# Optimization experiments

Measured on AMD Instinct MI355X. Metric: run time of the kernel, lower is better.

The kernel has to match this reference:

```python
import jax, jax.numpy as jnp
import numpy as np


def setup_inputs() -> dict:
    key = jax.random.key(0)
    k1, k2, k3, k4 = jax.random.split(key, 4)
    B, C_ORIG, H, W = 64, 448, 56, 56
    C = 100
    P = H * W
    feats = jax.random.normal(k1, (B, C_ORIG, H, W), dtype=jnp.float32)
    mean = jax.random.normal(k2, (P, C), dtype=jnp.float32)
    icov = jax.random.normal(k3, (P, C, C), dtype=jnp.float32)
    sel_idx = jnp.sort(jax.random.randint(k4, (C,), 0, C_ORIG, dtype=jnp.int64))
    return {"feats": feats, "mean": mean, "icov": icov, "sel_idx": sel_idx,
            "image_size": 224}


def reference(feats, mean, icov, sel_idx, image_size):
    # feats: [B, C_orig, H, W]; select the PaDiM random channel subset -> [B, C, H, W]
    f = feats[:, sel_idx]
    B, C, H, W = f.shape
    # [B, H*W, C] patch-major layout as in the torch code
    f = jnp.transpose(f, (0, 2, 3, 1)).reshape(B, H * W, C)
    # Per-patch Mahalanobis distance, fully batched over all H*W patches
    # (replaces the Python loop of H*W small einsums in the original).
    diff = f - mean[None]                                   # [B, P, C]
    dist = jnp.einsum('bpi,pij,bpj->bp', diff, icov, diff)  # [B, P]
    score_map = dist.reshape(B, H, W)
    # Bilinear upsample to input resolution (align_corners=False ~ half-pixel)
    score_map = jax.image.resize(score_map, (B, image_size, image_size),
                                 method='bilinear')
    return score_map
```

## Files before the change

### kernel.cpp

```cpp
#include <hip/hip_runtime.h>
#include <hip/hip_bf16.h>

#define B_N     64
#define C_ORIG  448
#define C_SEL   100
#define CP      128
#define HW      3136
#define IMG     224

typedef short bf16x8 __attribute__((ext_vector_type(8)));
typedef float f32x4  __attribute__((ext_vector_type(4)));

static __device__ __forceinline__ unsigned short f2bf(float f) {
    unsigned int u = __float_as_uint(f);
    return (unsigned short)((u + 0x7FFFu + ((u >> 16) & 1u)) >> 16);
}
static __device__ __forceinline__ float bf2f(unsigned short h) {
    return __uint_as_float(((unsigned int)h) << 16);
}

__global__ __launch_bounds__(256) void kA_gather(const float* __restrict__ feats,
                                                 const float* __restrict__ mean,
                                                 const int* __restrict__ sel,
                                                 unsigned short* __restrict__ D)
{
    __shared__ unsigned short Dt[64 * 128];
    char* DtB = reinterpret_cast<char*>(Dt);
    const int tid = threadIdx.x;
    const int p0  = blockIdx.x * 64;
    const int b   = blockIdx.y;

#pragma unroll
    for (int q = 0; q < 2; ++q) {
        int z = tid + q * 256;
        if (z < 448) {
            int pr = z / 7, un = 25 + z % 7;
            *reinterpret_cast<uint2*>(DtB + pr * 256 + ((8 * un) ^ ((pr & 31) << 3)))
                = make_uint2(0u, 0u);
        }
    }

    const int w    = tid >> 6;
    const int lane = tid & 63;
    const float* fb   = feats + (size_t)b * (C_ORIG * HW) + p0 + lane;
    const float* mrow = mean + (size_t)(p0 + lane) * C_SEL;
    const unsigned swz = (unsigned)(lane & 31) << 3;
    char* rowB = DtB + lane * 256;

    auto quad = [&](int c0) {
        int ch0 = sel[c0], ch1 = sel[c0 + 1], ch2 = sel[c0 + 2], ch3 = sel[c0 + 3];
        float4 m4 = *reinterpret_cast<const float4*>(mrow + c0);
        float v0 = fb[(size_t)ch0 * HW] - m4.x;
        float v1 = fb[(size_t)ch1 * HW] - m4.y;
        float v2 = fb[(size_t)ch2 * HW] - m4.z;
        float v3 = fb[(size_t)ch3 * HW] - m4.w;
        uint2 pk = make_uint2((unsigned)f2bf(v0) | ((unsigned)f2bf(v1) << 16),
                              (unsigned)f2bf(v2) | ((unsigned)f2bf(v3) << 16));
        *reinterpret_cast<uint2*>(rowB + (((unsigned)(2 * c0)) ^ swz)) = pk;
    };

    if (w < 3) {
#pragma unroll
        for (int q = 0; q < 6; ++q) quad(w * 24 + q * 4);
    } else {
#pragma unroll
        for (int q = 0; q < 7; ++q) quad(72 + q * 4);
    }
    __syncthreads();

    unsigned short* Dp = D + (size_t)p0 * (B_N * CP) + (size_t)b * CP;
#pragma unroll
    for (int q = 0; q < 4; ++q) {
        int unit = tid + q * 256;
        int pr = unit >> 4;
        int s  = unit & 15;
        unsigned off = ((unsigned)(16 * s)) ^ ((((unsigned)pr & 31u) << 3) & 0xF0u);
        uint4 v = *reinterpret_cast<const uint4*>(DtB + pr * 256 + off);
        uint4 r = (pr & 1) ? make_uint4(v.z, v.w, v.x, v.y) : v;
        *reinterpret_cast<uint4*>(reinterpret_cast<char*>(Dp)
            + (size_t)pr * (B_N * CP * 2) + s * 16) = r;
    }
}

__global__ __launch_bounds__(256) void kB_maha(const float* __restrict__ icov,
                                               const unsigned short* __restrict__ D,
                                               float* __restrict__ dist)
{
    __shared__ unsigned short Mb[112 * 128];
    char* MbB = reinterpret_cast<char*>(Mb);
    const int tid = threadIdx.x;
    const int p   = blockIdx.x;
    const int w    = tid >> 6;
    const int lane = tid & 63;
    const int lrow = lane & 15;
    const int g    = lane >> 4;
    const int bcol = w * 16 + lrow;
    const unsigned short* Drow = D + (size_t)p * (B_N * CP) + (size_t)bcol * CP;

    bf16x8 bfr[4];
#pragma unroll
    for (int ks = 0; ks < 4; ++ks)
        bfr[ks] = *reinterpret_cast<const bf16x8*>(Drow + ks * 32 + g * 8);
    ushort4 dvec[7];
#pragma unroll
    for (int it = 0; it < 7; ++it)
        dvec[it] = *reinterpret_cast<const ushort4*>(Drow + it * 16 + g * 4);

#pragma unroll
    for (int q = 0; q < 3; ++q) {
        int z = tid + q * 256;
        if (z < 700) {
            int i = z / 7, un = 25 + z % 7;
            *reinterpret_cast<uint2*>(MbB + i * 256 + ((8 * un) ^ ((i & 7) << 4)))
                = make_uint2(0u, 0u);
        }
    }
#pragma unroll
    for (int q = 0; q < 2; ++q) {
        int z = tid + q * 256;
        if (z < 384) {
            int i = 100 + (z >> 5), un = z & 31;
            *reinterpret_cast<uint2*>(MbB + i * 256 + ((8 * un) ^ ((i & 7) << 4)))
                = make_uint2(0u, 0u);
        }
    }
    const float4* src = reinterpret_cast<const float4*>(icov + (size_t)p * (C_SEL * C_SEL));
#pragma unroll
    for (int q = 0; q < 10; ++q) {
        int idx4 = tid + q * 256;
        if (idx4 < 2500) {
            float4 v = src[idx4];
            int i = idx4 / 25, un = idx4 % 25;
            uint2 pk = make_uint2((unsigned)f2bf(v.x) | ((unsigned)f2bf(v.y) << 16),
                                  (unsigned)f2bf(v.z) | ((unsigned)f2bf(v.w) << 16));
            *reinterpret_cast<uint2*>(MbB + i * 256 + ((8 * un) ^ ((i & 7) << 4))) = pk;
        }
    }
    __syncthreads();

    f32x4 acc[7];
#pragma unroll
    for (int it = 0; it < 7; ++it) acc[it] = (f32x4){0.f, 0.f, 0.f, 0.f};

#pragma unroll
    for (int ks = 0; ks < 4; ++ks) {
#pragma unroll
        for (int it = 0; it < 7; ++it) {
            int i = it * 16 + lrow;
            bf16x8 afrag = *reinterpret_cast<const bf16x8*>(
                MbB + i * 256 + ((ks * 64 + g * 16) ^ ((i & 7) << 4)));
            acc[it] = __builtin_amdgcn_mfma_f32_16x16x32_bf16(afrag, bfr[ks], acc[it], 0, 0, 0);
        }
    }

    float partial = 0.f;
#pragma unroll
    for (int it = 0; it < 7; ++it) {
#pragma unroll
        for (int r = 0; r < 4; ++r) {
            int i = it * 16 + g * 4 + r;
            if (i < C_SEL) {
                unsigned short dh = (r == 0) ? dvec[it].x : (r == 1) ? dvec[it].y
                                   : (r == 2) ? dvec[it].z : dvec[it].w;
                partial += acc[it][r] * bf2f(dh);
            }
        }
    }
    partial += __shfl_xor(partial, 16);
    partial += __shfl_xor(partial, 32);
    if (g == 0) dist[p * B_N + bcol] = partial;
}

__global__ __launch_bounds__(256) void kC_resize(const float* __restrict__ dist,
                                                 float* __restrict__ out)
{
    int gid = blockIdx.x * 256 + threadIdx.x;
    int m = gid % 56;
    int t = gid / 56;
    int y = t % IMG;
    int b = t / IMG;

    float sy = y * 0.25f - 0.375f;
    float fy0 = floorf(sy);
    float fy = sy - fy0;
    int y0 = max((int)fy0, 0);
    int y1 = min((int)fy0 + 1, 55);
    int xm1 = max(m - 1, 0);
    int xp1 = min(m + 1, 55);

    const float* d0 = dist + (y0 * 56) * B_N + b;
    const float* d1 = dist + (y1 * 56) * B_N + b;
    float a0 = d0[xm1 * B_N], b0 = d0[m * B_N], c0 = d0[xp1 * B_N];
    float a1 = d1[xm1 * B_N], b1 = d1[m * B_N], c1 = d1[xp1 * B_N];

    float A  = a0 + fy * (a1 - a0);
    float Bv = b0 + fy * (b1 - b0);
    float Cv = c0 + fy * (c1 - c0);

    float4 o;
    o.x = A  + 0.625f * (Bv - A);
    o.y = A  + 0.875f * (Bv - A);
    o.z = Bv + 0.125f * (Cv - Bv);
    o.w = Bv + 0.375f * (Cv - Bv);
    *reinterpret_cast<float4*>(out + ((size_t)b * IMG + y) * IMG + 4 * m) = o;
}

extern "C" void kernel_launch(void* const* d_in, const int* in_sizes, int n_in,
                              void* d_out, int out_size, void* d_ws, size_t ws_size,
                              hipStream_t stream)
{
    const float* feats = (const float*)d_in[0];
    const float* mean  = (const float*)d_in[1];
    const float* icov  = (const float*)d_in[2];
    const int*   sel   = (const int*)d_in[3];
    float* out = (float*)d_out;

    unsigned short* Dws = (unsigned short*)d_ws;
    float* distws = (float*)((char*)d_ws + (size_t)HW * B_N * CP * 2);

    dim3 gA(49, B_N);
    kA_gather<<<gA, 256, 0, stream>>>(feats, mean, sel, Dws);
    kB_maha<<<HW, 256, 0, stream>>>(icov, Dws, distws);
    kC_resize<<<3136, 256, 0, stream>>>(distws, out);
}
```

Before: 87.22 us.

## Load icov fragments directly into MFMA registers and shrink D padding

The Mahalanobis kernel no longer stages each patch's 100x100 icov into shared memory. Each lane now loads its own row fragments from global memory, converts them to bf16 in registers and feeds the MFMA directly, which removes the LDS fill, the barrier and the shared-memory footprint so more blocks fit per CU (launch bounds set to 4). The diff buffer padding drops from 128 to 112 channels to cut workspace traffic, and the distance output is stored batch-major so the resize kernel reads contiguous rows. In exchange, the icov global loads are less coalesced (per-lane 16-byte row pieces) and nothing overlaps them with compute.

```diff
diff --git a/kernel.cpp b/kernel.cpp
--- a/kernel.cpp
+++ b/kernel.cpp
@@ -4,16 +4,18 @@
 #define B_N     64
 #define C_ORIG  448
 #define C_SEL   100
-#define CP      128
+#define CPD     112
 #define HW      3136
 #define IMG     224
 
 typedef short bf16x8 __attribute__((ext_vector_type(8)));
 typedef float f32x4  __attribute__((ext_vector_type(4)));
-
-static __device__ __forceinline__ unsigned short f2bf(float f) {
-    unsigned int u = __float_as_uint(f);
-    return (unsigned short)((u + 0x7FFFu + ((u >> 16) & 1u)) >> 16);
+typedef unsigned int u32x4 __attribute__((ext_vector_type(4)));
+
+static __device__ __forceinline__ unsigned pkbf(float x, float y) {
+    union { __hip_bfloat162 h; unsigned u; } c;
+    c.h = __float22bfloat162_rn(float2{x, y});
+    return c.u;
 }
 static __device__ __forceinline__ float bf2f(unsigned short h) {
     return __uint_as_float(((unsigned int)h) << 16);
@@ -30,14 +32,10 @@
     const int p0  = blockIdx.x * 64;
     const int b   = blockIdx.y;
 
-#pragma unroll
-    for (int q = 0; q < 2; ++q) {
-        int z = tid + q * 256;
-        if (z < 448) {
-            int pr = z / 7, un = 25 + z % 7;
-            *reinterpret_cast<uint2*>(DtB + pr * 256 + ((8 * un) ^ ((pr & 31) << 3)))
-                = make_uint2(0u, 0u);
-        }
+    if (tid < 192) {
+        int pr = tid / 3, un = 25 + tid % 3;
+        *reinterpret_cast<uint2*>(DtB + pr * 256 + ((8 * un) ^ ((pr & 31) << 3)))
+            = make_uint2(0u, 0u);
     }
 
     const int w    = tid >> 6;
@@ -54,8 +52,7 @@
         float v1 = fb[(size_t)ch1 * HW] - m4.y;
         float v2 = fb[(size_t)ch2 * HW] - m4.z;
         float v3 = fb[(size_t)ch3 * HW] - m4.w;
-        uint2 pk = make_uint2((unsigned)f2bf(v0) | ((unsigned)f2bf(v1) << 16),
-                              (unsigned)f2bf(v2) | ((unsigned)f2bf(v3) << 16));
+        uint2 pk = make_uint2(pkbf(v0, v1), pkbf(v2, v3));
         *reinterpret_cast<uint2*>(rowB + (((unsigned)(2 * c0)) ^ swz)) = pk;
     };
 
@@ -68,34 +65,34 @@
     }
     __syncthreads();
 
-    unsigned short* Dp = D + (size_t)p0 * (B_N * CP) + (size_t)b * CP;
+    unsigned short* Dp = D + ((size_t)p0 * B_N + b) * CPD;
 #pragma unroll
     for (int q = 0; q < 4; ++q) {
         int unit = tid + q * 256;
-        int pr = unit >> 4;
-        int s  = unit & 15;
-        unsigned off = ((unsigned)(16 * s)) ^ ((((unsigned)pr & 31u) << 3) & 0xF0u);
-        uint4 v = *reinterpret_cast<const uint4*>(DtB + pr * 256 + off);
-        uint4 r = (pr & 1) ? make_uint4(v.z, v.w, v.x, v.y) : v;
-        *reinterpret_cast<uint4*>(reinterpret_cast<char*>(Dp)
-            + (size_t)pr * (B_N * CP * 2) + s * 16) = r;
-    }
-}
-
-__global__ __launch_bounds__(256) void kB_maha(const float* __restrict__ icov,
-                                               const unsigned short* __restrict__ D,
-                                               float* __restrict__ dist)
-{
-    __shared__ unsigned short Mb[112 * 128];
-    char* MbB = reinterpret_cast<char*>(Mb);
-    const int tid = threadIdx.x;
-    const int p   = blockIdx.x;
+        if (unit < 896) {
+            int pr = unit / 14;
+            int s  = unit % 14;
+            unsigned off = ((unsigned)(16 * s)) ^ ((((unsigned)pr & 31u) << 3) & 0xF0u);
+            uint4 v = *reinterpret_cast<const uint4*>(DtB + pr * 256 + off);
+            uint4 r = (pr & 1) ? make_uint4(v.z, v.w, v.x, v.y) : v;
+            *reinterpret_cast<uint4*>(reinterpret_cast<char*>(Dp)
+                + (size_t)pr * (B_N * CPD * 2) + s * 16) = r;
+        }
+    }
+}
+
+__global__ __launch_bounds__(256, 4) void kB_maha(const float* __restrict__ icov,
+                                                  const unsigned short* __restrict__ D,
+                                                  float* __restrict__ dist)
+{
+    const int tid  = threadIdx.x;
+    const int p    = blockIdx.x;
     const int w    = tid >> 6;
     const int lane = tid & 63;
     const int lrow = lane & 15;
     const int g    = lane >> 4;
     const int bcol = w * 16 + lrow;
-    const unsigned short* Drow = D + (size_t)p * (B_N * CP) + (size_t)bcol * CP;
+    const unsigned short* Drow = D + ((size_t)p * B_N + bcol) * CPD;
 
     bf16x8 bfr[4];
 #pragma unroll
@@ -106,50 +103,38 @@
     for (int it = 0; it < 7; ++it)
         dvec[it] = *reinterpret_cast<const ushort4*>(Drow + it * 16 + g * 4);
 
-#pragma unroll
-    for (int q = 0; q < 3; ++q) {
-        int z = tid + q * 256;
-        if (z < 700) {
-            int i = z / 7, un = 25 + z % 7;
-            *reinterpret_cast<uint2*>(MbB + i * 256 + ((8 * un) ^ ((i & 7) << 4)))
-                = make_uint2(0u, 0u);
-        }
-    }
-#pragma unroll
-    for (int q = 0; q < 2; ++q) {
-        int z = tid + q * 256;
-        if (z < 384) {
-            int i = 100 + (z >> 5), un = z & 31;
-            *reinterpret_cast<uint2*>(MbB + i * 256 + ((8 * un) ^ ((i & 7) << 4)))
-                = make_uint2(0u, 0u);
-        }
-    }
-    const float4* src = reinterpret_cast<const float4*>(icov + (size_t)p * (C_SEL * C_SEL));
-#pragma unroll
-    for (int q = 0; q < 10; ++q) {
-        int idx4 = tid + q * 256;
-        if (idx4 < 2500) {
-            float4 v = src[idx4];
-            int i = idx4 / 25, un = idx4 % 25;
-            uint2 pk = make_uint2((unsigned)f2bf(v.x) | ((unsigned)f2bf(v.y) << 16),
-                                  (unsigned)f2bf(v.z) | ((unsigned)f2bf(v.w) << 16));
-            *reinterpret_cast<uint2*>(MbB + i * 256 + ((8 * un) ^ ((i & 7) << 4))) = pk;
-        }
-    }
-    __syncthreads();
+    const float* Mp = icov + (size_t)p * (C_SEL * C_SEL);
 
     f32x4 acc[7];
 #pragma unroll
     for (int it = 0; it < 7; ++it) acc[it] = (f32x4){0.f, 0.f, 0.f, 0.f};
 
 #pragma unroll
-    for (int ks = 0; ks < 4; ++ks) {
-#pragma unroll
-        for (int it = 0; it < 7; ++it) {
-            int i = it * 16 + lrow;
-            bf16x8 afrag = *reinterpret_cast<const bf16x8*>(
-                MbB + i * 256 + ((ks * 64 + g * 16) ^ ((i & 7) << 4)));
-            acc[it] = __builtin_amdgcn_mfma_f32_16x16x32_bf16(afrag, bfr[ks], acc[it], 0, 0, 0);
+    for (int it = 0; it < 7; ++it) {
+        const int i = it * 16 + lrow;
+        const bool vr = (it < 6) || (lrow < 4);
+        const float* rowp = Mp + (size_t)i * C_SEL;
+#pragma unroll
+        for (int ks = 0; ks < 3; ++ks) {
+            float4 va = make_float4(0.f, 0.f, 0.f, 0.f), vb = va;
+            if (vr) {
+                va = *reinterpret_cast<const float4*>(rowp + ks * 32 + g * 8);
+                vb = *reinterpret_cast<const float4*>(rowp + ks * 32 + g * 8 + 4);
+            }
+            u32x4 u;
+            u[0] = pkbf(va.x, va.y); u[1] = pkbf(va.z, va.w);
+            u[2] = pkbf(vb.x, vb.y); u[3] = pkbf(vb.z, vb.w);
+            acc[it] = __builtin_amdgcn_mfma_f32_16x16x32_bf16(
+                __builtin_bit_cast(bf16x8, u), bfr[ks], acc[it], 0, 0, 0);
+        }
+        {
+            float4 va = make_float4(0.f, 0.f, 0.f, 0.f);
+            if (vr && g == 0) va = *reinterpret_cast<const float4*>(rowp + 96);
+            u32x4 u;
+            u[0] = pkbf(va.x, va.y); u[1] = pkbf(va.z, va.w);
+            u[2] = 0u; u[3] = 0u;
+            acc[it] = __builtin_amdgcn_mfma_f32_16x16x32_bf16(
+                __builtin_bit_cast(bf16x8, u), bfr[3], acc[it], 0, 0, 0);
         }
     }
 
@@ -168,7 +153,7 @@
     }
     partial += __shfl_xor(partial, 16);
     partial += __shfl_xor(partial, 32);
-    if (g == 0) dist[p * B_N + bcol] = partial;
+    if (g == 0) dist[(size_t)bcol * HW + p] = partial;
 }
 
 __global__ __launch_bounds__(256) void kC_resize(const float* __restrict__ dist,
@@ -188,10 +173,11 @@
     int xm1 = max(m - 1, 0);
     int xp1 = min(m + 1, 55);
 
-    const float* d0 = dist + (y0 * 56) * B_N + b;
-    const float* d1 = dist + (y1 * 56) * B_N + b;
-    float a0 = d0[xm1 * B_N], b0 = d0[m * B_N], c0 = d0[xp1 * B_N];
-    float a1 = d1[xm1 * B_N], b1 = d1[m * B_N], c1 = d1[xp1 * B_N];
+    const float* db = dist + (size_t)b * HW;
+    const float* d0 = db + y0 * 56;
+    const float* d1 = db + y1 * 56;
+    float a0 = d0[xm1], b0 = d0[m], c0 = d0[xp1];
+    float a1 = d1[xm1], b1 = d1[m], c1 = d1[xp1];
 
     float A  = a0 + fy * (a1 - a0);
     float Bv = b0 + fy * (b1 - b0);
@@ -216,7 +202,7 @@
     float* out = (float*)d_out;
 
     unsigned short* Dws = (unsigned short*)d_ws;
-    float* distws = (float*)((char*)d_ws + (size_t)HW * B_N * CP * 2);
+    float* distws = (float*)((char*)d_ws + (size_t)HW * B_N * CPD * 2);
 
     dim3 gA(49, B_N);
     kA_gather<<<gA, 256, 0, stream>>>(feats, mean, sel, Dws);
```

New measurement: 100.4 us. 15.1% more time.

## Shrink padded channel stride to 112 and make dist batch-major

Applied to the files above, without the earlier changes.

Reduces the per-row channel padding of the intermediate bf16 difference buffer from 128 to 112, cutting workspace write and read traffic between gather and Mahalanobis kernels. The score buffer is stored batch-major so the resize kernel reads contiguous neighbors. It also uses a packed bf16 conversion intrinsic and adds an occupancy hint to the MFMA kernel. The MFMA k-step still reads 128 entries per row, so the last 16 read past each row into neighboring data, relying on zeroed icov columns to cancel them.

```diff
diff --git a/kernel.cpp b/kernel.cpp
--- a/kernel.cpp
+++ b/kernel.cpp
@@ -4,16 +4,17 @@
 #define B_N     64
 #define C_ORIG  448
 #define C_SEL   100
-#define CP      128
+#define CPD     112
 #define HW      3136
 #define IMG     224
 
 typedef short bf16x8 __attribute__((ext_vector_type(8)));
 typedef float f32x4  __attribute__((ext_vector_type(4)));
 
-static __device__ __forceinline__ unsigned short f2bf(float f) {
-    unsigned int u = __float_as_uint(f);
-    return (unsigned short)((u + 0x7FFFu + ((u >> 16) & 1u)) >> 16);
+static __device__ __forceinline__ unsigned pkbf(float x, float y) {
+    union { __hip_bfloat162 h; unsigned u; } c;
+    c.h = __float22bfloat162_rn(float2{x, y});
+    return c.u;
 }
 static __device__ __forceinline__ float bf2f(unsigned short h) {
     return __uint_as_float(((unsigned int)h) << 16);
@@ -30,14 +31,10 @@
     const int p0  = blockIdx.x * 64;
     const int b   = blockIdx.y;
 
-#pragma unroll
-    for (int q = 0; q < 2; ++q) {
-        int z = tid + q * 256;
-        if (z < 448) {
-            int pr = z / 7, un = 25 + z % 7;
-            *reinterpret_cast<uint2*>(DtB + pr * 256 + ((8 * un) ^ ((pr & 31) << 3)))
-                = make_uint2(0u, 0u);
-        }
+    if (tid < 192) {
+        int pr = tid / 3, un = 25 + tid % 3;
+        *reinterpret_cast<uint2*>(DtB + pr * 256 + ((8 * un) ^ ((pr & 31) << 3)))
+            = make_uint2(0u, 0u);
     }
 
     const int w    = tid >> 6;
@@ -54,8 +51,7 @@
         float v1 = fb[(size_t)ch1 * HW] - m4.y;
         float v2 = fb[(size_t)ch2 * HW] - m4.z;
         float v3 = fb[(size_t)ch3 * HW] - m4.w;
-        uint2 pk = make_uint2((unsigned)f2bf(v0) | ((unsigned)f2bf(v1) << 16),
-                              (unsigned)f2bf(v2) | ((unsigned)f2bf(v3) << 16));
+        uint2 pk = make_uint2(pkbf(v0, v1), pkbf(v2, v3));
         *reinterpret_cast<uint2*>(rowB + (((unsigned)(2 * c0)) ^ swz)) = pk;
     };
 
@@ -68,34 +64,36 @@
     }
     __syncthreads();
 
-    unsigned short* Dp = D + (size_t)p0 * (B_N * CP) + (size_t)b * CP;
+    unsigned short* Dp = D + ((size_t)p0 * B_N + b) * CPD;
 #pragma unroll
     for (int q = 0; q < 4; ++q) {
         int unit = tid + q * 256;
-        int pr = unit >> 4;
-        int s  = unit & 15;
-        unsigned off = ((unsigned)(16 * s)) ^ ((((unsigned)pr & 31u) << 3) & 0xF0u);
-        uint4 v = *reinterpret_cast<const uint4*>(DtB + pr * 256 + off);
-        uint4 r = (pr & 1) ? make_uint4(v.z, v.w, v.x, v.y) : v;
-        *reinterpret_cast<uint4*>(reinterpret_cast<char*>(Dp)
-            + (size_t)pr * (B_N * CP * 2) + s * 16) = r;
-    }
-}
-
-__global__ __launch_bounds__(256) void kB_maha(const float* __restrict__ icov,
-                                               const unsigned short* __restrict__ D,
-                                               float* __restrict__ dist)
+        if (unit < 896) {
+            int pr = unit / 14;
+            int s  = unit % 14;
+            unsigned off = ((unsigned)(16 * s)) ^ ((((unsigned)pr & 31u) << 3) & 0xF0u);
+            uint4 v = *reinterpret_cast<const uint4*>(DtB + pr * 256 + off);
+            uint4 r = (pr & 1) ? make_uint4(v.z, v.w, v.x, v.y) : v;
+            *reinterpret_cast<uint4*>(reinterpret_cast<char*>(Dp)
+                + (size_t)pr * (B_N * CPD * 2) + s * 16) = r;
+        }
+    }
+}
+
+__global__ __launch_bounds__(256, 5) void kB_maha(const float* __restrict__ icov,
+                                                  const unsigned short* __restrict__ D,
+                                                  float* __restrict__ dist)
 {
     __shared__ unsigned short Mb[112 * 128];
     char* MbB = reinterpret_cast<char*>(Mb);
-    const int tid = threadIdx.x;
-    const int p   = blockIdx.x;
+    const int tid  = threadIdx.x;
+    const int p    = blockIdx.x;
     const int w    = tid >> 6;
     const int lane = tid & 63;
     const int lrow = lane & 15;
     const int g    = lane >> 4;
     const int bcol = w * 16 + lrow;
-    const unsigned short* Drow = D + (size_t)p * (B_N * CP) + (size_t)bcol * CP;
+    const unsigned short* Drow = D + ((size_t)p * B_N + bcol) * CPD;
 
     bf16x8 bfr[4];
 #pragma unroll
@@ -131,8 +129,7 @@
         if (idx4 < 2500) {
             float4 v = src[idx4];
             int i = idx4 / 25, un = idx4 % 25;
-            uint2 pk = make_uint2((unsigned)f2bf(v.x) | ((unsigned)f2bf(v.y) << 16),
-                                  (unsigned)f2bf(v.z) | ((unsigned)f2bf(v.w) << 16));
+            uint2 pk = make_uint2(pkbf(v.x, v.y), pkbf(v.z, v.w));
             *reinterpret_cast<uint2*>(MbB + i * 256 + ((8 * un) ^ ((i & 7) << 4))) = pk;
         }
     }
@@ -168,7 +165,7 @@
     }
     partial += __shfl_xor(partial, 16);
     partial += __shfl_xor(partial, 32);
-    if (g == 0) dist[p * B_N + bcol] = partial;
+    if (g == 0) dist[(size_t)bcol * HW + p] = partial;
 }
 
 __global__ __launch_bounds__(256) void kC_resize(const float* __restrict__ dist,
@@ -188,10 +185,11 @@
     int xm1 = max(m - 1, 0);
     int xp1 = min(m + 1, 55);
 
-    const float* d0 = dist + (y0 * 56) * B_N + b;
-    const float* d1 = dist + (y1 * 56) * B_N + b;
-    float a0 = d0[xm1 * B_N], b0 = d0[m * B_N], c0 = d0[xp1 * B_N];
-    float a1 = d1[xm1 * B_N], b1 = d1[m * B_N], c1 = d1[xp1 * B_N];
+    const float* db = dist + (size_t)b * HW;
+    const float* d0 = db + y0 * 56;
+    const float* d1 = db + y1 * 56;
+    float a0 = d0[xm1], b0 = d0[m], c0 = d0[xp1];
+    float a1 = d1[xm1], b1 = d1[m], c1 = d1[xp1];
 
     float A  = a0 + fy * (a1 - a0);
     float Bv = b0 + fy * (b1 - b0);
@@ -216,7 +214,7 @@
     float* out = (float*)d_out;
 
     unsigned short* Dws = (unsigned short*)d_ws;
-    float* distws = (float*)((char*)d_ws + (size_t)HW * B_N * CP * 2);
+    float* distws = (float*)((char*)d_ws + (size_t)HW * B_N * CPD * 2);
 
     dim3 gA(49, B_N);
     kA_gather<<<gA, 256, 0, stream>>>(feats, mean, sel, Dws);
```

Measured after the change: 78.42 us. -10.1%, faster.
